# Kernel optimization log

Measured on AMD Instinct MI355X. Metric: run time of the kernel, lower is better.

The kernel has to match this reference:

```python
import jax, jax.numpy as jnp
import numpy as np

B, T, N, F, H, R, E = 32, 8, 150, 16, 32, 4, 16


def _gconv(X, Af, Wf):
    # t-product graph conv (Kilmer t-product = circular conv over relation axis,
    # implemented facewise in the Fourier domain): ifft( fft(adj) @ fft(X) @ fft(W) )
    Xf = jnp.fft.fft(X, axis=-1)                      # [b,n,f,r] complex
    Y = jnp.einsum('nmr,bmfr->bnfr', Af, Xf)          # aggregate over nodes
    Y = jnp.einsum('bnfr,for->bnor', Y, Wf)           # feature transform
    return jnp.fft.ifft(Y, axis=-1).real


def _cell(X, Hs, Af, Wf, Bb):
    # TensorGRUCell. NOTE: faithful to the source, H_tilda reuses conv_hr
    # (conv_hh is defined but never used in the original forward).
    Wxz, Wxr, Wxh, Whz, Whr = Wf
    bz, br, bh = Bb[0], Bb[1], Bb[2]                  # [H,R], broadcasts over [b,n,H,R]
    Z = jax.nn.sigmoid(_gconv(X, Af, Wxz) + _gconv(Hs, Af, Whz) + bz)
    Rg = jax.nn.sigmoid(_gconv(X, Af, Wxr) + _gconv(Hs, Af, Whr) + br)
    Ht = jnp.tanh(_gconv(X, Af, Wxh) + _gconv(Rg * Hs, Af, Whr) + bh)
    return Z * Hs + (1.0 - Z) * Ht


def setup_inputs() -> dict:
    key = jax.random.key(0)
    ks = jax.random.split(key, 16)
    kai = lambda k, shp, fan: (jax.random.normal(k, shp, jnp.float32)
                               * np.float32(np.sqrt(2.0 / fan)))
    d = {}
    d['inputs'] = jax.random.normal(ks[0], (B, T, N, F, R), jnp.float32)
    d['U'] = kai(ks[1], (N, E, R), N)
    # layer 0 (input_dim=F)
    d['Wxz0'] = kai(ks[2], (F, H, R), F)
    d['Wxr0'] = kai(ks[3], (F, H, R), F)
    d['Wxh0'] = kai(ks[4], (F, H, R), F)
    d['Whz0'] = kai(ks[5], (H, H, R), H)
    d['Whr0'] = kai(ks[6], (H, H, R), H)
    d['B0'] = kai(ks[7], (3, H, R), 3)
    # layer 1 (input_dim=H)
    d['Wxz1'] = kai(ks[8], (H, H, R), H)
    d['Wxr1'] = kai(ks[9], (H, H, R), H)
    d['Wxh1'] = kai(ks[10], (H, H, R), H)
    d['Whz1'] = kai(ks[11], (H, H, R), H)
    d['Whr1'] = kai(ks[12], (H, H, R), H)
    d['B1'] = kai(ks[13], (3, H, R), 3)
    return d


def reference(inputs, U, Wxz0, Wxr0, Wxh0, Whz0, Whr0, B0,
              Wxz1, Wxr1, Wxh1, Whz1, Whr1, B1):
    # adaptive adjacency: softmax(relu(tprod(U, U^T)), dim=1)
    Uf = jnp.fft.fft(U, axis=-1)                      # [N,E,R] complex
    A = jnp.fft.ifft(jnp.einsum('ner,mer->nmr', Uf, Uf), axis=-1).real
    adj = jax.nn.softmax(jax.nn.relu(A), axis=1)      # [N,N,R]

    Af = jnp.fft.fft(adj, axis=-1)
    Wf0 = tuple(jnp.fft.fft(w, axis=-1) for w in (Wxz0, Wxr0, Wxh0, Whz0, Whr0))
    Wf1 = tuple(jnp.fft.fft(w, axis=-1) for w in (Wxz1, Wxr1, Wxh1, Whz1, Whr1))

    b, t, n, f, r = inputs.shape
    h = Whz0.shape[0]
    z0 = jnp.zeros((b, n, h, r), inputs.dtype)

    # t = 0: layer1 consumes the *current* layer0 output
    o0 = _cell(inputs[:, 0], z0, Af, Wf0, B0)
    o1 = _cell(o0, z0, Af, Wf1, B1)

    # t > 0: faithful to source, layer1 consumes the *previous timestep's*
    # layer0 output (temp_out[t-1][i-1]) with hidden temp_out[t-1][i].
    def step(carry, Xt):
        p0, p1 = carry
        n0 = _cell(Xt, p0, Af, Wf0, B0)
        n1 = _cell(p0, p1, Af, Wf1, B1)
        return (n0, n1), n1

    Xs = jnp.moveaxis(inputs[:, 1:], 1, 0)            # [T-1,B,N,F,R]
    (c0, c1), ys = jax.lax.scan(step, (o0, o1), Xs)

    out = jnp.concatenate([o1[None], ys], axis=0)     # [T,B,N,H,R]
    out = jnp.moveaxis(out, 0, 1)                     # [B,T,N,H,R]
    h_last = jnp.stack([c0, c1])                      # [L,B,N,H,R]
    return out, h_last
```

## Files before the change

### kernel.cpp

```cpp
#include <hip/hip_runtime.h>
#include <math.h>

#define NN 150
#define BB 32
#define TT 8
#define FF 16
#define HH 32
#define ROWS (NN*BB)
#define NCIN (BB*FF)
#define NCH  (BB*HH)
#define ADJ_LD 160
#define KPAD 68

#define SZ_ADJF (4*NN*ADJ_LD)
#define SZ_WA0  (4*48*32*4)
#define SZ_WA1  (4*64*32*4)
#define SZ_WB   (32*32*4)
#define SZ_STATE (ROWS*HH*4)
#define SZ_PIN  (4*NN*NCIN)

__device__ __forceinline__ float sigmoidf_(float x){ return 1.f/(1.f+expf(-x)); }

__device__ __forceinline__ float comp_of4(float x0, float x1, float x2, float x3, int c) {
  return c==0 ? (x0+x1+x2+x3) : c==1 ? (x0-x2) : c==2 ? (x3-x1) : (x0-x1+x2-x3);
}


__global__ __launch_bounds__(256) void k_adj(const float* __restrict__ U, float* __restrict__ adjF) {
  __shared__ float Ufl[NN*16*4];
  __shared__ float Arow[NN*4];
  __shared__ float red[256];
  __shared__ float mxs[4], isms[4];
  int n = blockIdx.x, tid = threadIdx.x;
  for (int idx = tid; idx < NN*16; idx += 256) {
    const float* s = U + (size_t)idx*4;
    float x0=s[0], x1=s[1], x2=s[2], x3=s[3];
    Ufl[idx*4+0] = x0+x1+x2+x3;
    Ufl[idx*4+1] = x0-x2;
    Ufl[idx*4+2] = x3-x1;
    Ufl[idx*4+3] = x0-x1+x2-x3;
  }
  __syncthreads();
  if (tid < NN) {
    int m = tid;
    float a0=0, ar=0, ai=0, a2=0;
    #pragma unroll
    for (int e = 0; e < 16; ++e) {
      const float* un = &Ufl[(n*16+e)*4];
      const float* um = &Ufl[(m*16+e)*4];
      a0 += un[0]*um[0];
      ar += un[1]*um[1] - un[2]*um[2];
      ai += un[1]*um[2] + un[2]*um[1];
      a2 += un[3]*um[3];
    }
    float r0 = 0.25f*(a0 + 2.f*ar + a2);
    float r1 = 0.25f*(a0 - 2.f*ai - a2);
    float r2 = 0.25f*(a0 - 2.f*ar + a2);
    float r3 = 0.25f*(a0 + 2.f*ai - a2);
    Arow[m*4+0] = fmaxf(r0, 0.f);
    Arow[m*4+1] = fmaxf(r1, 0.f);
    Arow[m*4+2] = fmaxf(r2, 0.f);
    Arow[m*4+3] = fmaxf(r3, 0.f);
  }
  __syncthreads();
  for (int r = 0; r < 4; ++r) {
    float v = (tid < NN) ? Arow[tid*4+r] : -1e30f;
    red[tid] = v; __syncthreads();
    for (int s = 128; s > 0; s >>= 1) { if (tid < s) red[tid] = fmaxf(red[tid], red[tid+s]); __syncthreads(); }
    if (tid == 0) mxs[r] = red[0];
    __syncthreads();
    float e = (tid < NN) ? expf(Arow[tid*4+r] - mxs[r]) : 0.f;
    red[tid] = e; __syncthreads();
    for (int s = 128; s > 0; s >>= 1) { if (tid < s) red[tid] += red[tid+s]; __syncthreads(); }
    if (tid == 0) isms[r] = 1.f / red[0];
    __syncthreads();
    if (tid < NN) Arow[tid*4+r] = e * isms[r];
    __syncthreads();
  }
  if (tid < NN) {
    int m = tid;
    float e0=Arow[m*4+0], e1=Arow[m*4+1], e2=Arow[m*4+2], e3=Arow[m*4+3];
    size_t base = (size_t)n*ADJ_LD + m;
    size_t cs = (size_t)NN*ADJ_LD;
    adjF[base]      = e0+e1+e2+e3;
    adjF[base+cs]   = e0-e2;
    adjF[base+2*cs] = e3-e1;
    adjF[base+3*cs] = e0-e1+e2-e3;
  } else if (tid < ADJ_LD) {
    size_t base = (size_t)n*ADJ_LD + tid;
    size_t cs = (size_t)NN*ADJ_LD;
    adjF[base] = 0.f; adjF[base+cs] = 0.f; adjF[base+2*cs] = 0.f; adjF[base+3*cs] = 0.f;
  }
}

__global__ __launch_bounds__(256) void k_wts(
    const float* __restrict__ Wxz0, const float* __restrict__ Wxr0, const float* __restrict__ Wxh0,
    const float* __restrict__ Whz0, const float* __restrict__ Whr0,
    const float* __restrict__ Wxz1, const float* __restrict__ Wxr1, const float* __restrict__ Wxh1,
    const float* __restrict__ Whz1, const float* __restrict__ Whr1,
    float* __restrict__ WA0p, float* __restrict__ WA1p,
    float* __restrict__ WB0p, float* __restrict__ WB1p) {
  int idx = blockIdx.x*256 + threadIdx.x;
  const float* src = nullptr;
  float* dst; int didx; int c;
  if (idx < SZ_WA0) {
    c = idx / 6144;
    int rem = idx % 6144;
    int k = rem >> 7, og = (rem >> 2) & 31, q = rem & 3;
    if (q == 0) src = (k < FF) ? Wxz0 + ((size_t)k*HH + og)*4 : Whz0 + ((size_t)(k-FF)*HH + og)*4;
    else if (q == 1) src = (k < FF) ? Wxr0 + ((size_t)k*HH + og)*4 : Whr0 + ((size_t)(k-FF)*HH + og)*4;
    else if (q == 2 && k < FF) src = Wxh0 + ((size_t)k*HH + og)*4;
    dst = WA0p; didx = idx;
  } else if (idx < SZ_WA0 + SZ_WA1) {
    int id = idx - SZ_WA0;
    c = id >> 13;
    int rem = id & 8191;
    int k = rem >> 7, og = (rem >> 2) & 31, q = rem & 3;
    if (q == 0) src = (k < HH) ? Wxz1 + ((size_t)k*HH + og)*4 : Whz1 + ((size_t)(k-HH)*HH + og)*4;
    else if (q == 1) src = (k < HH) ? Wxr1 + ((size_t)k*HH + og)*4 : Whr1 + ((size_t)(k-HH)*HH + og)*4;
    else if (q == 2 && k < HH) src = Wxh1 + ((size_t)k*HH + og)*4;
    dst = WA1p; didx = id;
  } else if (idx < SZ_WA0 + SZ_WA1 + SZ_WB) {
    int id = idx - (SZ_WA0 + SZ_WA1);
    int k = id >> 7, o = (id >> 2) & 31;
    c = id & 3;
    src = Whr0 + ((size_t)k*HH + o)*4;
    dst = WB0p; didx = id;
  } else if (idx < SZ_WA0 + SZ_WA1 + 2*SZ_WB) {
    int id = idx - (SZ_WA0 + SZ_WA1 + SZ_WB);
    int k = id >> 7, o = (id >> 2) & 31;
    c = id & 3;
    src = Whr1 + ((size_t)k*HH + o)*4;
    dst = WB1p; didx = id;
  } else return;
  float v0=0,v1=0,v2=0,v3=0;
  if (src) { v0=src[0]; v1=src[1]; v2=src[2]; v3=src[3]; }
  dst[didx] = comp_of4(v0,v1,v2,v3,c);
}

struct AggParams {
  const float* X0; const float* X1; const float* X2;
  float* P0; float* P1; float* P2;
  int ncol0, ncol1, ncol2;
  int base1, base2, njobs, rawt, nb;
};
__global__ __launch_bounds__(256,4) void k_agg(AggParams pr, const float* __restrict__ adjF,
                                               const float* __restrict__ inp) {
  __shared__ float As[4*32*37];
  __shared__ float Xs[4*32*36];
  int bid = blockIdx.x;
  int part = (bid >= pr.nb) ? 1 : 0;
  if (part) bid -= pr.nb;
  const float* X; float* P; int ncol; int tile; bool raw = false;
  if (pr.njobs >= 3 && bid >= pr.base2) { X = pr.X2; P = pr.P2; ncol = pr.ncol2; tile = bid - pr.base2; }
  else if (pr.njobs >= 2 && bid >= pr.base1) { X = pr.X1; P = pr.P1; ncol = pr.ncol1; tile = bid - pr.base1; }
  else { X = pr.X0; P = pr.P0; ncol = pr.ncol0; tile = bid; raw = (pr.rawt >= 0); }
  P += (size_t)part * 4 * NN * ncol;
  int kbeg = part ? 96 : 0;
  int kend = part ? NN : 96;
  int n0 = (tile % 5) * 32;
  int col0 = (tile / 5) * 32;
  int tid = threadIdx.x;
  int ti = tid & 31, tj = tid >> 5;
  int j0 = tj * 4;
  float a0[4]={}, aR[4]={}, aI[4]={}, a2v[4]={};

  float4 pa[4];
  float4 px[4];

  #define LOAD_A(K0)                                                         \
    _Pragma("unroll")                                                        \
    for (int u = 0; u < 4; ++u) {                                            \
      int e = tid + u*256;                                                   \
      int c = e >> 8, rem = e & 255, i = rem >> 3, kq = rem & 7;             \
      int nn_ = n0 + i;                                                      \
      pa[u] = make_float4(0,0,0,0);                                          \
      if (nn_ < NN) pa[u] = *(const float4*)(adjF + ((size_t)c*NN + nn_)*ADJ_LD + (K0) + kq*4); \
    }
  #define STORE_A()                                                          \
    _Pragma("unroll")                                                        \
    for (int u = 0; u < 4; ++u) {                                            \
      int e = tid + u*256;                                                   \
      int c = e >> 8, rem = e & 255, i = rem >> 3, kq = rem & 7;             \
      As[(c*32 + kq*4+0)*37 + i] = pa[u].x;                                  \
      As[(c*32 + kq*4+1)*37 + i] = pa[u].y;                                  \
      As[(c*32 + kq*4+2)*37 + i] = pa[u].z;                                  \
      As[(c*32 + kq*4+3)*37 + i] = pa[u].w;                                  \
    }
  #define LOAD_X(K0)                                                         \
    if (raw) {                                                               \
      int q = tid & 7, kk = tid >> 3;                                        \
      int mm = (K0) + kk;                                                    \
      int col = col0 + q*4;                                                  \
      int b = col >> 4, f = col & 15;                                        \
      px[0]=px[1]=px[2]=px[3]=make_float4(0,0,0,0);                          \
      if (mm < NN) {                                                         \
        const float* s = inp + (((size_t)(b*TT + pr.rawt)*NN + mm)*FF + f)*4;\
        px[0] = *(const float4*)(s+0);                                       \
        px[1] = *(const float4*)(s+4);                                       \
        px[2] = *(const float4*)(s+8);                                       \
        px[3] = *(const float4*)(s+12);                                      \
      }                                                                      \
    } else {                                                                 \
      _Pragma("unroll")                                                      \
      for (int u = 0; u < 4; ++u) {                                          \
        int e = tid + u*256;                                                 \
        int c = e >> 8, rem = e & 255, kk = rem >> 3, q = rem & 7;           \
        int mm = (K0) + kk;                                                  \
        px[u] = make_float4(0,0,0,0);                                        \
        if (mm < NN) px[u] = *(const float4*)(X + ((size_t)c*NN + mm)*ncol + col0 + q*4); \
      }                                                                      \
    }
  #define STORE_X()                                                          \
    if (raw) {                                                               \
      int q = tid & 7, kk = tid >> 3;                                        \
      float4 r0 = px[0], r1 = px[1], r2 = px[2], r3 = px[3];                 \
      float4 w;                                                              \
      w = make_float4(r0.x+r0.y+r0.z+r0.w, r1.x+r1.y+r1.z+r1.w, r2.x+r2.y+r2.z+r2.w, r3.x+r3.y+r3.z+r3.w); \
      *(float4*)&Xs[(0*32+kk)*36 + q*4] = w;                                 \
      w = make_float4(r0.x-r0.z, r1.x-r1.z, r2.x-r2.z, r3.x-r3.z);           \
      *(float4*)&Xs[(1*32+kk)*36 + q*4] = w;                                 \
      w = make_float4(r0.w-r0.y, r1.w-r1.y, r2.w-r2.y, r3.w-r3.y);           \
      *(float4*)&Xs[(2*32+kk)*36 + q*4] = w;                                 \
      w = make_float4(r0.x-r0.y+r0.z-r0.w, r1.x-r1.y+r1.z-r1.w, r2.x-r2.y+r2.z-r2.w, r3.x-r3.y+r3.z-r3.w); \
      *(float4*)&Xs[(3*32+kk)*36 + q*4] = w;                                 \
    } else {                                                                 \
      _Pragma("unroll")                                                      \
      for (int u = 0; u < 4; ++u) {                                          \
        int e = tid + u*256;                                                 \
        int c = e >> 8, rem = e & 255, kk = rem >> 3, q = rem & 7;           \
        *(float4*)&Xs[(c*32+kk)*36 + q*4] = px[u];                           \
      }                                                                      \
    }

  LOAD_A(kbeg)
  LOAD_X(kbeg)
  for (int k0 = kbeg; k0 < kend; k0 += 32) {
    STORE_A()
    STORE_X()
    __syncthreads();
    int k0n = k0 + 32;
    if (k0n < kend) {
      LOAD_A(k0n)
      LOAD_X(k0n)
    }
    #pragma unroll 4
    for (int k = 0; k < 32; ++k) {
      float A0 = As[(0*32+k)*37 + ti];
      float A1 = As[(1*32+k)*37 + ti];
      float A2 = As[(2*32+k)*37 + ti];
      float A3 = As[(3*32+k)*37 + ti];
      float4 x0 = *(float4*)&Xs[(0*32+k)*36 + j0];
      float4 x1 = *(float4*)&Xs[(1*32+k)*36 + j0];
      float4 x2 = *(float4*)&Xs[(2*32+k)*36 + j0];
      float4 x3 = *(float4*)&Xs[(3*32+k)*36 + j0];
      float X0v[4]={x0.x,x0.y,x0.z,x0.w}, X1v[4]={x1.x,x1.y,x1.z,x1.w};
      float X2v[4]={x2.x,x2.y,x2.z,x2.w}, X3v[4]={x3.x,x3.y,x3.z,x3.w};
      #pragma unroll
      for (int j = 0; j < 4; ++j) {
        a0[j] += A0*X0v[j];
        aR[j] += A1*X1v[j] - A2*X2v[j];
        aI[j] += A1*X2v[j] + A2*X1v[j];
        a2v[j] += A3*X3v[j];
      }
    }
    __syncthreads();
  }
  int nn_ = n0 + ti;
  if (nn_ < NN) {
    size_t cs = (size_t)NN*ncol;
    size_t rb = (size_t)nn_*ncol + col0 + j0;
    *(float4*)&P[rb]      = make_float4(a0[0],a0[1],a0[2],a0[3]);
    *(float4*)&P[rb+cs]   = make_float4(aR[0],aR[1],aR[2],aR[3]);
    *(float4*)&P[rb+2*cs] = make_float4(aI[0],aI[1],aI[2],aI[3]);
    *(float4*)&P[rb+3*cs] = make_float4(a2v[0],a2v[1],a2v[2],a2v[3]);
  }
}

struct FAJob {
  const float* Px;
  const float* Ph;
  const float* W;
  const float* bias;
  const float* hprev;
  float* Z; float* T1; float* Mf;
  int zh;
};
struct FAParams { FAJob j[2]; };

template<int KTOT, int KX>
__device__ __forceinline__ void fusedA_body(const FAJob& jb, float* Ps, float* Ws) {
  const int row0 = blockIdx.x * 16;
  const int tid = threadIdx.x;
  const int og = tid & 31;
  const int rg = tid >> 5;
  const int r0 = rg*2, r1 = rg*2 + 1;
  const size_t psx = (size_t)4*ROWS*KX;
  const size_t psh = (size_t)4*ROWS*HH;
  constexpr int K4 = KTOT/4;
  for (int e = tid; e < 16*4*K4; e += 256) {
    int k4 = e % K4; int c = (e / K4) & 3; int r = e / (K4*4);
    int k = k4*4;
    int row = row0 + r;
    float4 v;
    if (k < KX) {
      const float* a = &jb.Px[((size_t)c*ROWS + row)*KX + k];
      float4 va = *(const float4*)a;
      float4 vb = *(const float4*)(a + psx);
      v = make_float4(va.x+vb.x, va.y+vb.y, va.z+vb.z, va.w+vb.w);
    } else if (jb.zh) {
      v = make_float4(0,0,0,0);
    } else {
      const float* a = &jb.Ph[((size_t)c*ROWS + row)*HH + (k - KX)];
      float4 va = *(const float4*)a;
      float4 vb = *(const float4*)(a + psh);
      v = make_float4(va.x+vb.x, va.y+vb.y, va.z+vb.z, va.w+vb.w);
    }
    *(float4*)&Ps[(r*4 + c)*KPAD + k] = v;
  }
  float acc0[2][3]={{0,0,0},{0,0,0}}, accR[2][3]={{0,0,0},{0,0,0}};
  float accI[2][3]={{0,0,0},{0,0,0}}, acc2[2][3]={{0,0,0},{0,0,0}};
  constexpr int NCHK = KTOT/16;
  const float4* Wg = (const float4*)jb.W;
  for (int cc = 0; cc < NCHK; ++cc) {
    __syncthreads();
    #pragma unroll
    for (int u = 0; u < 8; ++u) {
      int f = tid + u*256;
      int c = f >> 9, rem = f & 511;
      float4 v = Wg[((size_t)c*KTOT + cc*16)*32 + rem];
      *(float4*)&Ws[((size_t)c*512 + rem)*4] = v;
    }
    __syncthreads();
    #pragma unroll 4
    for (int kk = 0; kk < 16; ++kk) {
      int k = cc*16 + kk;
      float p0a = Ps[(r0*4+0)*KPAD + k];
      float p1a = Ps[(r0*4+1)*KPAD + k];
      float p2a = Ps[(r0*4+2)*KPAD + k];
      float p3a = Ps[(r0*4+3)*KPAD + k];
      float p0b = Ps[(r1*4+0)*KPAD + k];
      float p1b = Ps[(r1*4+1)*KPAD + k];
      float p2b = Ps[(r1*4+2)*KPAD + k];
      float p3b = Ps[(r1*4+3)*KPAD + k];
      float4 w0 = *(float4*)&Ws[((0*16+kk)*32+og)*4];
      float4 w1 = *(float4*)&Ws[((1*16+kk)*32+og)*4];
      float4 w2 = *(float4*)&Ws[((2*16+kk)*32+og)*4];
      float4 w3 = *(float4*)&Ws[((3*16+kk)*32+og)*4];
      float W0v[3]={w0.x,w0.y,w0.z}, W1v[3]={w1.x,w1.y,w1.z};
      float W2v[3]={w2.x,w2.y,w2.z}, W3v[3]={w3.x,w3.y,w3.z};
      #pragma unroll
      for (int q = 0; q < 3; ++q) {
        acc0[0][q] += p0a*W0v[q];
        acc0[1][q] += p0b*W0v[q];
        accR[0][q] += p1a*W1v[q] - p2a*W2v[q];
        accR[1][q] += p1b*W1v[q] - p2b*W2v[q];
        accI[0][q] += p1a*W2v[q] + p2a*W1v[q];
        accI[1][q] += p1b*W2v[q] + p2b*W1v[q];
        acc2[0][q] += p3a*W3v[q];
        acc2[1][q] += p3b*W3v[q];
      }
    }
  }
  const float* bz = jb.bias + (0*HH + og)*4;
  const float* br = jb.bias + (1*HH + og)*4;
  const float* bh = jb.bias + (2*HH + og)*4;
  float bzv[4] = {bz[0],bz[1],bz[2],bz[3]};
  float brv[4] = {br[0],br[1],br[2],br[3]};
  float bhv[4] = {bh[0],bh[1],bh[2],bh[3]};
  #pragma unroll
  for (int rr = 0; rr < 2; ++rr) {
    int row = row0 + rg*2 + rr;
    float ys[3][4];
    #pragma unroll
    for (int q = 0; q < 3; ++q) {
      float Y0 = acc0[rr][q], Yr = accR[rr][q], Yi = accI[rr][q], Y2 = acc2[rr][q];
      ys[q][0] = 0.25f*(Y0 + 2.f*Yr + Y2);
      ys[q][1] = 0.25f*(Y0 - 2.f*Yi - Y2);
      ys[q][2] = 0.25f*(Y0 - 2.f*Yr + Y2);
      ys[q][3] = 0.25f*(Y0 + 2.f*Yi - Y2);
    }
    float4 z = make_float4(sigmoidf_(ys[0][0]+bzv[0]), sigmoidf_(ys[0][1]+bzv[1]),
                           sigmoidf_(ys[0][2]+bzv[2]), sigmoidf_(ys[0][3]+bzv[3]));
    *(float4*)&jb.Z[((size_t)row*HH + og)*4] = z;
    float4 hp = make_float4(0,0,0,0);
    if (!jb.zh) hp = *(const float4*)&jb.hprev[((size_t)row*HH + og)*4];
    float m0 = sigmoidf_(ys[1][0]+brv[0]) * hp.x;
    float m1 = sigmoidf_(ys[1][1]+brv[1]) * hp.y;
    float m2 = sigmoidf_(ys[1][2]+brv[2]) * hp.z;
    float m3 = sigmoidf_(ys[1][3]+brv[3]) * hp.w;
    size_t mb = (size_t)row*HH + og;
    size_t cs = (size_t)ROWS*HH;
    jb.Mf[mb]      = m0+m1+m2+m3;
    jb.Mf[mb+cs]   = m0-m2;
    jb.Mf[mb+2*cs] = m3-m1;
    jb.Mf[mb+3*cs] = m0-m1+m2-m3;
    float4 tv = make_float4(ys[2][0]+bhv[0], ys[2][1]+bhv[1], ys[2][2]+bhv[2], ys[2][3]+bhv[3]);
    *(float4*)&jb.T1[((size_t)row*HH + og)*4] = tv;
  }
}

__global__ __launch_bounds__(256,3) void k_fusedA_both(FAParams pr) {
  __shared__ float Ps[16*4*KPAD];
  __shared__ float Ws[8192];
  if (blockIdx.y == 0) fusedA_body<48,16>(pr.j[0], Ps, Ws);
  else                 fusedA_body<64,32>(pr.j[1], Ps, Ws);
}
__global__ __launch_bounds__(256,3) void k_fusedA_L0(FAParams pr) {
  __shared__ float Ps[16*4*KPAD];
  __shared__ float Ws[8192];
  fusedA_body<48,16>(pr.j[0], Ps, Ws);
}
__global__ __launch_bounds__(256,3) void k_fusedA_L1(FAParams pr) {
  __shared__ float Ps[16*4*KPAD];
  __shared__ float Ws[8192];
  fusedA_body<64,32>(pr.j[1], Ps, Ws);
}

struct FBJob {
  const float* Pm; const float* W; const float* T1; const float* Z;
  float* h; float* hf; float* outp; float* hlast;
  int t, zh, wout;
};
struct FBParams { FBJob j[2]; };
__global__ __launch_bounds__(256,4) void k_fusedB(FBParams pr) {
  __shared__ float Ps[16*32*4];
  __shared__ float Ws[32*32*4];
  FBJob jb = pr.j[blockIdx.y];
  int row0 = blockIdx.x * 16;
  int tid = threadIdx.x;
  int rg = tid >> 5, o = tid & 31;
  int r0 = rg*2, r1 = r0 + 1;
  float acc0[2]={0,0}, accR[2]={0,0}, accI[2]={0,0}, acc2[2]={0,0};
  if (!jb.zh) {
    #pragma unroll
    for (int u = 0; u < 4; ++u) {
      int f = tid + u*256;
      ((float4*)Ws)[f] = ((const float4*)jb.W)[f];
    }
    const size_t psh = (size_t)4*ROWS*HH;
    #pragma unroll
    for (int u = 0; u < 2; ++u) {
      int e = tid + u*256;
      int r = e >> 5, k = e & 31;
      int row = row0 + r;
      float4 v;
      float* vv = (float*)&v;
      #pragma unroll
      for (int c = 0; c < 4; ++c) {
        size_t ix = ((size_t)c*ROWS + row)*HH + k;
        vv[c] = jb.Pm[ix] + jb.Pm[ix + psh];
      }
      *(float4*)&Ps[(r*32 + k)*4] = v;
    }
    __syncthreads();
    #pragma unroll 8
    for (int k = 0; k < 32; ++k) {
      float4 pA = *(const float4*)&Ps[(r0*32 + k)*4];
      float4 pB = *(const float4*)&Ps[(r1*32 + k)*4];
      float4 w  = *(const float4*)&Ws[(k*32 + o)*4];
      acc0[0] += pA.x*w.x;  acc0[1] += pB.x*w.x;
      accR[0] += pA.y*w.y - pA.z*w.z;  accR[1] += pB.y*w.y - pB.z*w.z;
      accI[0] += pA.y*w.z + pA.z*w.y;  accI[1] += pB.y*w.z + pB.z*w.y;
      acc2[0] += pA.w*w.w;  acc2[1] += pB.w*w.w;
    }
  }
  #pragma unroll
  for (int rr = 0; rr < 2; ++rr) {
    int row = row0 + rg*2 + rr;
    float y0 = 0.25f*(acc0[rr] + 2.f*accR[rr] + acc2[rr]);
    float y1 = 0.25f*(acc0[rr] - 2.f*accI[rr] - acc2[rr]);
    float y2 = 0.25f*(acc0[rr] - 2.f*accR[rr] + acc2[rr]);
    float y3 = 0.25f*(acc0[rr] + 2.f*accI[rr] - acc2[rr]);
    float4 t1 = *(const float4*)&jb.T1[((size_t)row*HH + o)*4];
    float h0v = tanhf(t1.x + y0);
    float h1v = tanhf(t1.y + y1);
    float h2v = tanhf(t1.z + y2);
    float h3v = tanhf(t1.w + y3);
    float4 z = *(const float4*)&jb.Z[((size_t)row*HH + o)*4];
    float4 hp = make_float4(0,0,0,0);
    if (!jb.zh) hp = *(const float4*)&jb.h[((size_t)row*HH + o)*4];
    float n0v = z.x*hp.x + (1.f-z.x)*h0v;
    float n1v = z.y*hp.y + (1.f-z.y)*h1v;
    float n2v = z.z*hp.z + (1.f-z.z)*h2v;
    float n3v = z.w*hp.w + (1.f-z.w)*h3v;
    *(float4*)&jb.h[((size_t)row*HH + o)*4] = make_float4(n0v,n1v,n2v,n3v);
    size_t hb = (size_t)row*HH + o, cs = (size_t)ROWS*HH;
    jb.hf[hb]      = n0v+n1v+n2v+n3v;
    jb.hf[hb+cs]   = n0v-n2v;
    jb.hf[hb+2*cs] = n3v-n1v;
    jb.hf[hb+3*cs] = n0v-n1v+n2v-n3v;
    int n = row >> 5, b = row & 31;
    if (jb.wout) {
      float* dst = jb.outp + (((size_t)b*TT + jb.t)*NN + n)*(HH*4) + o*4;
      *(float4*)dst = make_float4(n0v,n1v,n2v,n3v);
    }
    if (jb.hlast) {
      float* dst = jb.hlast + ((size_t)(b*NN + n))*(HH*4) + o*4;
      *(float4*)dst = make_float4(n0v,n1v,n2v,n3v);
    }
  }
}

extern "C" void kernel_launch(void* const* d_in, const int* in_sizes, int n_in,
                              void* d_out, int out_size, void* d_ws, size_t ws_size,
                              hipStream_t stream) {
  const float* inp  = (const float*)d_in[0];
  const float* U    = (const float*)d_in[1];
  const float* Wxz0 = (const float*)d_in[2];
  const float* Wxr0 = (const float*)d_in[3];
  const float* Wxh0 = (const float*)d_in[4];
  const float* Whz0 = (const float*)d_in[5];
  const float* Whr0 = (const float*)d_in[6];
  const float* B0   = (const float*)d_in[7];
  const float* Wxz1 = (const float*)d_in[8];
  const float* Wxr1 = (const float*)d_in[9];
  const float* Wxh1 = (const float*)d_in[10];
  const float* Whz1 = (const float*)d_in[11];
  const float* Whr1 = (const float*)d_in[12];
  const float* B1   = (const float*)d_in[13];
  float* out = (float*)d_out;

  float* ws = (float*)d_ws;
  float* ADJF = ws;  ws += SZ_ADJF;
  float* WA0  = ws;  ws += SZ_WA0;
  float* WA1  = ws;  ws += SZ_WA1;
  float* WB0  = ws;  ws += SZ_WB;
  float* WB1  = ws;  ws += SZ_WB;
  float* H0   = ws;  ws += SZ_STATE;
  float* H1   = ws;  ws += SZ_STATE;
  float* H0F  = ws;  ws += SZ_STATE;
  float* H1F  = ws;  ws += SZ_STATE;
  float* PIN  = ws;  ws += 2*SZ_PIN;
  float* PH0  = ws;  ws += 2*SZ_STATE;
  float* PH1  = ws;  ws += 2*SZ_STATE;
  float* PM0  = ws;  ws += 2*SZ_STATE;
  float* PM1  = ws;  ws += 2*SZ_STATE;
  float* M0F  = ws;  ws += SZ_STATE;
  float* M1F  = ws;  ws += SZ_STATE;
  float* Z0   = ws;  ws += SZ_STATE;
  float* Z1   = ws;  ws += SZ_STATE;
  float* T10  = ws;  ws += SZ_STATE;
  float* T11  = ws;  ws += SZ_STATE;

  k_adj<<<NN, 256, 0, stream>>>(U, ADJF);
  k_wts<<<(SZ_WA0+SZ_WA1+2*SZ_WB+255)/256, 256, 0, stream>>>(
      Wxz0,Wxr0,Wxh0,Whz0,Whr0,Wxz1,Wxr1,Wxh1,Whz1,Whr1,WA0,WA1,WB0,WB1);

  {
    AggParams p; p.X0=nullptr; p.P0=PIN; p.ncol0=NCIN;
    p.X1=nullptr; p.P1=nullptr; p.ncol1=0; p.X2=nullptr; p.P2=nullptr; p.ncol2=0;
    p.base1=0; p.base2=0; p.njobs=1; p.rawt=0; p.nb=80;
    k_agg<<<160, 256, 0, stream>>>(p, ADJF, inp);
  }
  {
    FAParams p;
    p.j[0] = FAJob{PIN, nullptr, WA0, B0, nullptr, Z0, T10, M0F, 1};
    p.j[1] = p.j[0];
    k_fusedA_L0<<<dim3(300,1), 256, 0, stream>>>(p);
  }
  {
    FBParams p;
    p.j[0] = FBJob{nullptr, WB0, T10, Z0, H0, H0F, nullptr, nullptr, 0, 1, 0};
    p.j[1] = p.j[0];
    k_fusedB<<<dim3(300,1), 256, 0, stream>>>(p);
  }
  {
    AggParams p; p.X0=H0F; p.P0=PH0; p.ncol0=NCH;
    p.X1=nullptr; p.P1=nullptr; p.ncol1=0; p.X2=nullptr; p.P2=nullptr; p.ncol2=0;
    p.base1=0; p.base2=0; p.njobs=1; p.rawt=-1; p.nb=160;
    k_agg<<<320, 256, 0, stream>>>(p, ADJF, inp);
  }
  {
    FAParams p;
    p.j[0] = FAJob{PH0, nullptr, WA1, B1, nullptr, Z1, T11, M1F, 1};
    p.j[1] = p.j[0];
    k_fusedA_L1<<<dim3(300,1), 256, 0, stream>>>(p);
  }
  {
    FBParams p;
    p.j[0] = FBJob{nullptr, WB1, T11, Z1, H1, H1F, out, nullptr, 0, 1, 1};
    p.j[1] = p.j[0];
    k_fusedB<<<dim3(300,1), 256, 0, stream>>>(p);
  }

  float* hlast0 = out + (size_t)BB*TT*NN*HH*4;
  float* hlast1 = hlast0 + (size_t)BB*NN*HH*4;
  for (int t = 1; t < TT; ++t) {
    {
      AggParams p;
      p.X0=nullptr; p.P0=PIN; p.ncol0=NCIN;
      p.X1=H0F; p.P1=PH0; p.ncol1=NCH;
      p.X2=H1F; p.P2=PH1; p.ncol2=NCH;
      p.base1=80; p.base2=240; p.njobs=3; p.rawt=t; p.nb=400;
      k_agg<<<800, 256, 0, stream>>>(p, ADJF, inp);
    }
    {
      FAParams p;
      p.j[0] = FAJob{PIN, PH0, WA0, B0, H0, Z0, T10, M0F, 0};
      p.j[1] = FAJob{PH0, PH1, WA1, B1, H1, Z1, T11, M1F, 0};
      k_fusedA_both<<<dim3(300,2), 256, 0, stream>>>(p);
    }
    {
      AggParams p;
      p.X0=M0F; p.P0=PM0; p.ncol0=NCH;
      p.X1=M1F; p.P1=PM1; p.ncol1=NCH;
      p.X2=nullptr; p.P2=nullptr; p.ncol2=0;
      p.base1=160; p.base2=0; p.njobs=2; p.rawt=-1; p.nb=320;
      k_agg<<<640, 256, 0, stream>>>(p, ADJF, inp);
    }
    {
      int last = (t == TT-1);
      FBParams p;
      p.j[0] = FBJob{PM0, WB0, T10, Z0, H0, H0F, nullptr, last ? hlast0 : nullptr, t, 0, 0};
      p.j[1] = FBJob{PM1, WB1, T11, Z1, H1, H1F, out,     last ? hlast1 : nullptr, t, 0, 1};
      k_fusedB<<<dim3(300,2), 256, 0, stream>>>(p);
    }
  }
}
```

Baseline: 846.2 us.

## Fuse recurrent timestep kernels into persistent megakernel with grid barriers

Replaces the roughly thirty small per-timestep launches with one persistent kernel. Its blocks loop over work units for each stage and synchronise through atomic-counter grid barriers. The input aggregation for all timesteps is hoisted into one up-front kernel, and the adjacency and weight preprocessing kernels are merged into one launch. The aim is to remove launch overhead and the idle tails between dependent stages. In exchange it relies on all blocks being co-resident: the grid is sized from an occupancy query, and a miscount would deadlock. Spin-wait barriers also add their own latency at each stage.

```diff
diff --git a/kernel.cpp b/kernel.cpp
--- a/kernel.cpp
+++ b/kernel.cpp
@@ -26,81 +26,83 @@
 }
 
 
-__global__ __launch_bounds__(256) void k_adj(const float* __restrict__ U, float* __restrict__ adjF) {
-  __shared__ float Ufl[NN*16*4];
-  __shared__ float Arow[NN*4];
-  __shared__ float red[256];
-  __shared__ float mxs[4], isms[4];
-  int n = blockIdx.x, tid = threadIdx.x;
-  for (int idx = tid; idx < NN*16; idx += 256) {
-    const float* s = U + (size_t)idx*4;
-    float x0=s[0], x1=s[1], x2=s[2], x3=s[3];
-    Ufl[idx*4+0] = x0+x1+x2+x3;
-    Ufl[idx*4+1] = x0-x2;
-    Ufl[idx*4+2] = x3-x1;
-    Ufl[idx*4+3] = x0-x1+x2-x3;
-  }
-  __syncthreads();
-  if (tid < NN) {
-    int m = tid;
-    float a0=0, ar=0, ai=0, a2=0;
-    #pragma unroll
-    for (int e = 0; e < 16; ++e) {
-      const float* un = &Ufl[(n*16+e)*4];
-      const float* um = &Ufl[(m*16+e)*4];
-      a0 += un[0]*um[0];
-      ar += un[1]*um[1] - un[2]*um[2];
-      ai += un[1]*um[2] + un[2]*um[1];
-      a2 += un[3]*um[3];
-    }
-    float r0 = 0.25f*(a0 + 2.f*ar + a2);
-    float r1 = 0.25f*(a0 - 2.f*ai - a2);
-    float r2 = 0.25f*(a0 - 2.f*ar + a2);
-    float r3 = 0.25f*(a0 + 2.f*ai - a2);
-    Arow[m*4+0] = fmaxf(r0, 0.f);
-    Arow[m*4+1] = fmaxf(r1, 0.f);
-    Arow[m*4+2] = fmaxf(r2, 0.f);
-    Arow[m*4+3] = fmaxf(r3, 0.f);
-  }
-  __syncthreads();
-  for (int r = 0; r < 4; ++r) {
-    float v = (tid < NN) ? Arow[tid*4+r] : -1e30f;
-    red[tid] = v; __syncthreads();
-    for (int s = 128; s > 0; s >>= 1) { if (tid < s) red[tid] = fmaxf(red[tid], red[tid+s]); __syncthreads(); }
-    if (tid == 0) mxs[r] = red[0];
-    __syncthreads();
-    float e = (tid < NN) ? expf(Arow[tid*4+r] - mxs[r]) : 0.f;
-    red[tid] = e; __syncthreads();
-    for (int s = 128; s > 0; s >>= 1) { if (tid < s) red[tid] += red[tid+s]; __syncthreads(); }
-    if (tid == 0) isms[r] = 1.f / red[0];
-    __syncthreads();
-    if (tid < NN) Arow[tid*4+r] = e * isms[r];
-    __syncthreads();
-  }
-  if (tid < NN) {
-    int m = tid;
-    float e0=Arow[m*4+0], e1=Arow[m*4+1], e2=Arow[m*4+2], e3=Arow[m*4+3];
-    size_t base = (size_t)n*ADJ_LD + m;
-    size_t cs = (size_t)NN*ADJ_LD;
-    adjF[base]      = e0+e1+e2+e3;
-    adjF[base+cs]   = e0-e2;
-    adjF[base+2*cs] = e3-e1;
-    adjF[base+3*cs] = e0-e1+e2-e3;
-  } else if (tid < ADJ_LD) {
-    size_t base = (size_t)n*ADJ_LD + tid;
-    size_t cs = (size_t)NN*ADJ_LD;
-    adjF[base] = 0.f; adjF[base+cs] = 0.f; adjF[base+2*cs] = 0.f; adjF[base+3*cs] = 0.f;
-  }
-}
-
-__global__ __launch_bounds__(256) void k_wts(
+__global__ __launch_bounds__(256) void k_pre(
+    const float* __restrict__ U, float* __restrict__ adjF,
     const float* __restrict__ Wxz0, const float* __restrict__ Wxr0, const float* __restrict__ Wxh0,
     const float* __restrict__ Whz0, const float* __restrict__ Whr0,
     const float* __restrict__ Wxz1, const float* __restrict__ Wxr1, const float* __restrict__ Wxh1,
     const float* __restrict__ Whz1, const float* __restrict__ Whr1,
     float* __restrict__ WA0p, float* __restrict__ WA1p,
     float* __restrict__ WB0p, float* __restrict__ WB1p) {
-  int idx = blockIdx.x*256 + threadIdx.x;
+  __shared__ float Ufl[NN*16*4];
+  __shared__ float Arow[NN*4];
+  __shared__ float red[256];
+  __shared__ float mxs[4], isms[4];
+  int tid = threadIdx.x;
+  if (blockIdx.x < NN) {
+    int n = blockIdx.x;
+    for (int idx = tid; idx < NN*16; idx += 256) {
+      const float* s = U + (size_t)idx*4;
+      float x0=s[0], x1=s[1], x2=s[2], x3=s[3];
+      Ufl[idx*4+0] = x0+x1+x2+x3;
+      Ufl[idx*4+1] = x0-x2;
+      Ufl[idx*4+2] = x3-x1;
+      Ufl[idx*4+3] = x0-x1+x2-x3;
+    }
+    __syncthreads();
+    if (tid < NN) {
+      int m = tid;
+      float a0=0, ar=0, ai=0, a2=0;
+      #pragma unroll
+      for (int e = 0; e < 16; ++e) {
+        const float* un = &Ufl[(n*16+e)*4];
+        const float* um = &Ufl[(m*16+e)*4];
+        a0 += un[0]*um[0];
+        ar += un[1]*um[1] - un[2]*um[2];
+        ai += un[1]*um[2] + un[2]*um[1];
+        a2 += un[3]*um[3];
+      }
+      float r0 = 0.25f*(a0 + 2.f*ar + a2);
+      float r1 = 0.25f*(a0 - 2.f*ai - a2);
+      float r2 = 0.25f*(a0 - 2.f*ar + a2);
+      float r3 = 0.25f*(a0 + 2.f*ai - a2);
+      Arow[m*4+0] = fmaxf(r0, 0.f);
+      Arow[m*4+1] = fmaxf(r1, 0.f);
+      Arow[m*4+2] = fmaxf(r2, 0.f);
+      Arow[m*4+3] = fmaxf(r3, 0.f);
+    }
+    __syncthreads();
+    for (int r = 0; r < 4; ++r) {
+      float v = (tid < NN) ? Arow[tid*4+r] : -1e30f;
+      red[tid] = v; __syncthreads();
+      for (int s = 128; s > 0; s >>= 1) { if (tid < s) red[tid] = fmaxf(red[tid], red[tid+s]); __syncthreads(); }
+      if (tid == 0) mxs[r] = red[0];
+      __syncthreads();
+      float e = (tid < NN) ? expf(Arow[tid*4+r] - mxs[r]) : 0.f;
+      red[tid] = e; __syncthreads();
+      for (int s = 128; s > 0; s >>= 1) { if (tid < s) red[tid] += red[tid+s]; __syncthreads(); }
+      if (tid == 0) isms[r] = 1.f / red[0];
+      __syncthreads();
+      if (tid < NN) Arow[tid*4+r] = e * isms[r];
+      __syncthreads();
+    }
+    if (tid < NN) {
+      int m = tid;
+      float e0=Arow[m*4+0], e1=Arow[m*4+1], e2=Arow[m*4+2], e3=Arow[m*4+3];
+      size_t base = (size_t)n*ADJ_LD + m;
+      size_t cs = (size_t)NN*ADJ_LD;
+      adjF[base]      = e0+e1+e2+e3;
+      adjF[base+cs]   = e0-e2;
+      adjF[base+2*cs] = e3-e1;
+      adjF[base+3*cs] = e0-e1+e2-e3;
+    } else if (tid < ADJ_LD) {
+      size_t base = (size_t)n*ADJ_LD + tid;
+      size_t cs = (size_t)NN*ADJ_LD;
+      adjF[base] = 0.f; adjF[base+cs] = 0.f; adjF[base+2*cs] = 0.f; adjF[base+3*cs] = 0.f;
+    }
+    return;
+  }
+  int idx = (blockIdx.x - NN)*256 + tid;
   const float* src = nullptr;
   float* dst; int didx; int c;
   if (idx < SZ_WA0) {
@@ -138,35 +140,21 @@
   dst[didx] = comp_of4(v0,v1,v2,v3,c);
 }
 
-struct AggParams {
-  const float* X0; const float* X1; const float* X2;
-  float* P0; float* P1; float* P2;
-  int ncol0, ncol1, ncol2;
-  int base1, base2, njobs, rawt, nb;
-};
-__global__ __launch_bounds__(256,4) void k_agg(AggParams pr, const float* __restrict__ adjF,
-                                               const float* __restrict__ inp) {
-  __shared__ float As[4*32*37];
-  __shared__ float Xs[4*32*36];
-  int bid = blockIdx.x;
-  int part = (bid >= pr.nb) ? 1 : 0;
-  if (part) bid -= pr.nb;
-  const float* X; float* P; int ncol; int tile; bool raw = false;
-  if (pr.njobs >= 3 && bid >= pr.base2) { X = pr.X2; P = pr.P2; ncol = pr.ncol2; tile = bid - pr.base2; }
-  else if (pr.njobs >= 2 && bid >= pr.base1) { X = pr.X1; P = pr.P1; ncol = pr.ncol1; tile = bid - pr.base1; }
-  else { X = pr.X0; P = pr.P0; ncol = pr.ncol0; tile = bid; raw = (pr.rawt >= 0); }
-  P += (size_t)part * 4 * NN * ncol;
+template<bool RAW>
+__device__ __forceinline__ void agg_body(const float* __restrict__ adjF,
+                                         const float* __restrict__ X,
+                                         const float* __restrict__ inp,
+                                         float* __restrict__ P, int ncol,
+                                         int tile, int part, int rawt,
+                                         float* As, float* Xs, int tid) {
   int kbeg = part ? 96 : 0;
   int kend = part ? NN : 96;
   int n0 = (tile % 5) * 32;
   int col0 = (tile / 5) * 32;
-  int tid = threadIdx.x;
   int ti = tid & 31, tj = tid >> 5;
   int j0 = tj * 4;
   float a0[4]={}, aR[4]={}, aI[4]={}, a2v[4]={};
-
-  float4 pa[4];
-  float4 px[4];
+  float4 pa[4], px[4];
 
   #define LOAD_A(K0)                                                         \
     _Pragma("unroll")                                                        \
@@ -188,14 +176,14 @@
       As[(c*32 + kq*4+3)*37 + i] = pa[u].w;                                  \
     }
   #define LOAD_X(K0)                                                         \
-    if (raw) {                                                               \
+    if (RAW) {                                                               \
       int q = tid & 7, kk = tid >> 3;                                        \
       int mm = (K0) + kk;                                                    \
       int col = col0 + q*4;                                                  \
       int b = col >> 4, f = col & 15;                                        \
       px[0]=px[1]=px[2]=px[3]=make_float4(0,0,0,0);                          \
       if (mm < NN) {                                                         \
-        const float* s = inp + (((size_t)(b*TT + pr.rawt)*NN + mm)*FF + f)*4;\
+        const float* s = inp + (((size_t)(b*TT + rawt)*NN + mm)*FF + f)*4;   \
         px[0] = *(const float4*)(s+0);                                       \
         px[1] = *(const float4*)(s+4);                                       \
         px[2] = *(const float4*)(s+8);                                       \
@@ -212,7 +200,7 @@
       }                                                                      \
     }
   #define STORE_X()                                                          \
-    if (raw) {                                                               \
+    if (RAW) {                                                               \
       int q = tid & 7, kk = tid >> 3;                                        \
       float4 r0 = px[0], r1 = px[1], r2 = px[2], r3 = px[3];                 \
       float4 w;                                                              \
@@ -266,6 +254,10 @@
     }
     __syncthreads();
   }
+  #undef LOAD_A
+  #undef STORE_A
+  #undef LOAD_X
+  #undef STORE_X
   int nn_ = n0 + ti;
   if (nn_ < NN) {
     size_t cs = (size_t)NN*ncol;
@@ -275,6 +267,17 @@
     *(float4*)&P[rb+2*cs] = make_float4(aI[0],aI[1],aI[2],aI[3]);
     *(float4*)&P[rb+3*cs] = make_float4(a2v[0],a2v[1],a2v[2],a2v[3]);
   }
+}
+
+__global__ __launch_bounds__(256,4) void k_aggIN(const float* __restrict__ adjF,
+                                                 const float* __restrict__ inp,
+                                                 float* __restrict__ PIN) {
+  __shared__ float As[4736];
+  __shared__ float Xs[4608];
+  int u = blockIdx.x;
+  int t = u / 160, rem = u % 160, part = rem / 80, tile = rem % 80;
+  float* P = PIN + (size_t)t*2*SZ_PIN + (size_t)part*SZ_PIN;
+  agg_body<true>(adjF, nullptr, inp, P, NCIN, tile, part, t, As, Xs, threadIdx.x);
 }
 
 struct FAJob {
@@ -286,12 +289,11 @@
   float* Z; float* T1; float* Mf;
   int zh;
 };
-struct FAParams { FAJob j[2]; };
 
 template<int KTOT, int KX>
-__device__ __forceinline__ void fusedA_body(const FAJob& jb, float* Ps, float* Ws) {
-  const int row0 = blockIdx.x * 16;
-  const int tid = threadIdx.x;
+__device__ __forceinline__ void fusedA_unit(const FAJob& jb, float* Ps, float* Ws, int unit, int tid) {
+  __syncthreads();
+  const int row0 = unit * 16;
   const int og = tid & 31;
   const int rg = tid >> 5;
   const int r0 = rg*2, r1 = rg*2 + 1;
@@ -400,35 +402,15 @@
   }
 }
 
-__global__ __launch_bounds__(256,3) void k_fusedA_both(FAParams pr) {
-  __shared__ float Ps[16*4*KPAD];
-  __shared__ float Ws[8192];
-  if (blockIdx.y == 0) fusedA_body<48,16>(pr.j[0], Ps, Ws);
-  else                 fusedA_body<64,32>(pr.j[1], Ps, Ws);
-}
-__global__ __launch_bounds__(256,3) void k_fusedA_L0(FAParams pr) {
-  __shared__ float Ps[16*4*KPAD];
-  __shared__ float Ws[8192];
-  fusedA_body<48,16>(pr.j[0], Ps, Ws);
-}
-__global__ __launch_bounds__(256,3) void k_fusedA_L1(FAParams pr) {
-  __shared__ float Ps[16*4*KPAD];
-  __shared__ float Ws[8192];
-  fusedA_body<64,32>(pr.j[1], Ps, Ws);
-}
-
 struct FBJob {
   const float* Pm; const float* W; const float* T1; const float* Z;
   float* h; float* hf; float* outp; float* hlast;
   int t, zh, wout;
 };
-struct FBParams { FBJob j[2]; };
-__global__ __launch_bounds__(256,4) void k_fusedB(FBParams pr) {
-  __shared__ float Ps[16*32*4];
-  __shared__ float Ws[32*32*4];
-  FBJob jb = pr.j[blockIdx.y];
-  int row0 = blockIdx.x * 16;
-  int tid = threadIdx.x;
+
+__device__ __forceinline__ void fusedB_unit(const FBJob& jb, float* Ps, float* Ws, int unit, int tid) {
+  __syncthreads();
+  int row0 = unit * 16;
   int rg = tid >> 5, o = tid & 31;
   int r0 = rg*2, r1 = r0 + 1;
   float acc0[2]={0,0}, accR[2]={0,0}, accI[2]={0,0}, acc2[2]={0,0};
@@ -502,6 +484,104 @@
   }
 }
 
+__device__ __forceinline__ void gbar(int* cnt, int idx, int nblk) {
+  __syncthreads();
+  if (threadIdx.x == 0) {
+    __threadfence();
+    atomicAdd(&cnt[idx], 1);
+    while (__hip_atomic_load(&cnt[idx], __ATOMIC_RELAXED, __HIP_MEMORY_SCOPE_AGENT) < nblk) {
+      __builtin_amdgcn_s_sleep(2);
+    }
+    __threadfence();
+  }
+  __syncthreads();
+}
+
+struct MegaParams {
+  const float* adjF; const float* PIN;
+  const float* WA0; const float* WA1; const float* WB0; const float* WB1;
+  const float* B0; const float* B1;
+  float* H0; float* H1; float* H0F; float* H1F;
+  float* PH0; float* PH1; float* PM0; float* PM1;
+  float* M0F; float* M1F; float* Z0; float* Z1; float* T10; float* T11;
+  float* out; float* hlast0; float* hlast1;
+  int* cnt; int nblk;
+};
+
+__global__ __launch_bounds__(256,3) void k_mega(MegaParams mp) {
+  __shared__ float smem[12544];
+  const int tid = threadIdx.x;
+  const int bid = blockIdx.x;
+  const int gsz = gridDim.x;
+  int bslot = 0;
+
+  for (int u = bid; u < 300; u += gsz) {
+    FAJob jb{mp.PIN, nullptr, mp.WA0, mp.B0, nullptr, mp.Z0, mp.T10, mp.M0F, 1};
+    fusedA_unit<48,16>(jb, smem, smem+4352, u, tid);
+  }
+  gbar(mp.cnt, bslot++, mp.nblk);
+  for (int u = bid; u < 300; u += gsz) {
+    FBJob jb{nullptr, mp.WB0, mp.T10, mp.Z0, mp.H0, mp.H0F, nullptr, nullptr, 0, 1, 0};
+    fusedB_unit(jb, smem, smem+2048, u, tid);
+  }
+  gbar(mp.cnt, bslot++, mp.nblk);
+  for (int u = bid; u < 320; u += gsz) {
+    int part = u / 160, tile = u % 160;
+    agg_body<false>(mp.adjF, mp.H0F, nullptr, mp.PH0 + (size_t)part*SZ_STATE, NCH, tile, part, -1,
+                    smem, smem+4736, tid);
+  }
+  gbar(mp.cnt, bslot++, mp.nblk);
+  for (int u = bid; u < 300; u += gsz) {
+    FAJob jb{mp.PH0, nullptr, mp.WA1, mp.B1, nullptr, mp.Z1, mp.T11, mp.M1F, 1};
+    fusedA_unit<64,32>(jb, smem, smem+4352, u, tid);
+  }
+  gbar(mp.cnt, bslot++, mp.nblk);
+  for (int u = bid; u < 300; u += gsz) {
+    FBJob jb{nullptr, mp.WB1, mp.T11, mp.Z1, mp.H1, mp.H1F, mp.out, nullptr, 0, 1, 1};
+    fusedB_unit(jb, smem, smem+2048, u, tid);
+  }
+  gbar(mp.cnt, bslot++, mp.nblk);
+
+  for (int t = 1; t < TT; ++t) {
+    const float* PINt = mp.PIN + (size_t)t * 2 * SZ_PIN;
+    for (int u = bid; u < 640; u += gsz) {
+      int job = u / 320, rem = u % 320, part = rem / 160, tile = rem % 160;
+      const float* X = job ? mp.H1F : mp.H0F;
+      float* P = (job ? mp.PH1 : mp.PH0) + (size_t)part*SZ_STATE;
+      agg_body<false>(mp.adjF, X, nullptr, P, NCH, tile, part, -1, smem, smem+4736, tid);
+    }
+    gbar(mp.cnt, bslot++, mp.nblk);
+    for (int u = bid; u < 600; u += gsz) {
+      if (u < 300) {
+        FAJob jb{PINt, mp.PH0, mp.WA0, mp.B0, mp.H0, mp.Z0, mp.T10, mp.M0F, 0};
+        fusedA_unit<48,16>(jb, smem, smem+4352, u, tid);
+      } else {
+        FAJob jb{mp.PH0, mp.PH1, mp.WA1, mp.B1, mp.H1, mp.Z1, mp.T11, mp.M1F, 0};
+        fusedA_unit<64,32>(jb, smem, smem+4352, u-300, tid);
+      }
+    }
+    gbar(mp.cnt, bslot++, mp.nblk);
+    for (int u = bid; u < 640; u += gsz) {
+      int job = u / 320, rem = u % 320, part = rem / 160, tile = rem % 160;
+      const float* X = job ? mp.M1F : mp.M0F;
+      float* P = (job ? mp.PM1 : mp.PM0) + (size_t)part*SZ_STATE;
+      agg_body<false>(mp.adjF, X, nullptr, P, NCH, tile, part, -1, smem, smem+4736, tid);
+    }
+    gbar(mp.cnt, bslot++, mp.nblk);
+    int last = (t == TT-1);
+    for (int u = bid; u < 600; u += gsz) {
+      if (u < 300) {
+        FBJob jb{mp.PM0, mp.WB0, mp.T10, mp.Z0, mp.H0, mp.H0F, nullptr, last ? mp.hlast0 : nullptr, t, 0, 0};
+        fusedB_unit(jb, smem, smem+2048, u, tid);
+      } else {
+        FBJob jb{mp.PM1, mp.WB1, mp.T11, mp.Z1, mp.H1, mp.H1F, mp.out, last ? mp.hlast1 : nullptr, t, 0, 1};
+        fusedB_unit(jb, smem, smem+2048, u-300, tid);
+      }
+    }
+    if (!last) gbar(mp.cnt, bslot++, mp.nblk);
+  }
+}
+
 extern "C" void kernel_launch(void* const* d_in, const int* in_sizes, int n_in,
                               void* d_out, int out_size, void* d_ws, size_t ws_size,
                               hipStream_t stream) {
@@ -531,7 +611,7 @@
   float* H1   = ws;  ws += SZ_STATE;
   float* H0F  = ws;  ws += SZ_STATE;
   float* H1F  = ws;  ws += SZ_STATE;
-  float* PIN  = ws;  ws += 2*SZ_PIN;
+  float* PIN  = ws;  ws += (size_t)TT*2*SZ_PIN;
   float* PH0  = ws;  ws += 2*SZ_STATE;
   float* PH1  = ws;  ws += 2*SZ_STATE;
   float* PM0  = ws;  ws += 2*SZ_STATE;
@@ -542,79 +622,32 @@
   float* Z1   = ws;  ws += SZ_STATE;
   float* T10  = ws;  ws += SZ_STATE;
   float* T11  = ws;  ws += SZ_STATE;
-
-  k_adj<<<NN, 256, 0, stream>>>(U, ADJF);
-  k_wts<<<(SZ_WA0+SZ_WA1+2*SZ_WB+255)/256, 256, 0, stream>>>(
-      Wxz0,Wxr0,Wxh0,Whz0,Whr0,Wxz1,Wxr1,Wxh1,Whz1,Whr1,WA0,WA1,WB0,WB1);
-
-  {
-    AggParams p; p.X0=nullptr; p.P0=PIN; p.ncol0=NCIN;
-    p.X1=nullptr; p.P1=nullptr; p.ncol1=0; p.X2=nullptr; p.P2=nullptr; p.ncol2=0;
-    p.base1=0; p.base2=0; p.njobs=1; p.rawt=0; p.nb=80;
-    k_agg<<<160, 256, 0, stream>>>(p, ADJF, inp);
-  }
-  {
-    FAParams p;
-    p.j[0] = FAJob{PIN, nullptr, WA0, B0, nullptr, Z0, T10, M0F, 1};
-    p.j[1] = p.j[0];
-    k_fusedA_L0<<<dim3(300,1), 256, 0, stream>>>(p);
-  }
-  {
-    FBParams p;
-    p.j[0] = FBJob{nullptr, WB0, T10, Z0, H0, H0F, nullptr, nullptr, 0, 1, 0};
-    p.j[1] = p.j[0];
-    k_fusedB<<<dim3(300,1), 256, 0, stream>>>(p);
-  }
-  {
-    AggParams p; p.X0=H0F; p.P0=PH0; p.ncol0=NCH;
-    p.X1=nullptr; p.P1=nullptr; p.ncol1=0; p.X2=nullptr; p.P2=nullptr; p.ncol2=0;
-    p.base1=0; p.base2=0; p.njobs=1; p.rawt=-1; p.nb=160;
-    k_agg<<<320, 256, 0, stream>>>(p, ADJF, inp);
-  }
-  {
-    FAParams p;
-    p.j[0] = FAJob{PH0, nullptr, WA1, B1, nullptr, Z1, T11, M1F, 1};
-    p.j[1] = p.j[0];
-    k_fusedA_L1<<<dim3(300,1), 256, 0, stream>>>(p);
-  }
-  {
-    FBParams p;
-    p.j[0] = FBJob{nullptr, WB1, T11, Z1, H1, H1F, out, nullptr, 0, 1, 1};
-    p.j[1] = p.j[0];
-    k_fusedB<<<dim3(300,1), 256, 0, stream>>>(p);
-  }
-
-  float* hlast0 = out + (size_t)BB*TT*NN*HH*4;
-  float* hlast1 = hlast0 + (size_t)BB*NN*HH*4;
-  for (int t = 1; t < TT; ++t) {
-    {
-      AggParams p;
-      p.X0=nullptr; p.P0=PIN; p.ncol0=NCIN;
-      p.X1=H0F; p.P1=PH0; p.ncol1=NCH;
-      p.X2=H1F; p.P2=PH1; p.ncol2=NCH;
-      p.base1=80; p.base2=240; p.njobs=3; p.rawt=t; p.nb=400;
-      k_agg<<<800, 256, 0, stream>>>(p, ADJF, inp);
-    }
-    {
-      FAParams p;
-      p.j[0] = FAJob{PIN, PH0, WA0, B0, H0, Z0, T10, M0F, 0};
-      p.j[1] = FAJob{PH0, PH1, WA1, B1, H1, Z1, T11, M1F, 0};
-      k_fusedA_both<<<dim3(300,2), 256, 0, stream>>>(p);
-    }
-    {
-      AggParams p;
-      p.X0=M0F; p.P0=PM0; p.ncol0=NCH;
-      p.X1=M1F; p.P1=PM1; p.ncol1=NCH;
-      p.X2=nullptr; p.P2=nullptr; p.ncol2=0;
-      p.base1=160; p.base2=0; p.njobs=2; p.rawt=-1; p.nb=320;
-      k_agg<<<640, 256, 0, stream>>>(p, ADJF, inp);
-    }
-    {
-      int last = (t == TT-1);
-      FBParams p;
-      p.j[0] = FBJob{PM0, WB0, T10, Z0, H0, H0F, nullptr, last ? hlast0 : nullptr, t, 0, 0};
-      p.j[1] = FBJob{PM1, WB1, T11, Z1, H1, H1F, out,     last ? hlast1 : nullptr, t, 0, 1};
-      k_fusedB<<<dim3(300,2), 256, 0, stream>>>(p);
-    }
-  }
-}
+  int*   CNT  = (int*)ws; ws += 64;
+
+  hipMemsetAsync(CNT, 0, 64*sizeof(int), stream);
+
+  k_pre<<<NN + (SZ_WA0+SZ_WA1+2*SZ_WB+255)/256, 256, 0, stream>>>(
+      U, ADJF, Wxz0,Wxr0,Wxh0,Whz0,Whr0, Wxz1,Wxr1,Wxh1,Whz1,Whr1, WA0,WA1,WB0,WB1);
+
+  k_aggIN<<<TT*2*80, 256, 0, stream>>>(ADJF, inp, PIN);
+
+  int nbPerCU = 0;
+  if (hipOccupancyMaxActiveBlocksPerMultiprocessor(&nbPerCU, k_mega, 256, 0) != hipSuccess || nbPerCU <= 0)
+    nbPerCU = 2;
+  int grid = nbPerCU * 256;
+  if (grid > 640) grid = 640;
+
+  MegaParams mp;
+  mp.adjF = ADJF; mp.PIN = PIN;
+  mp.WA0 = WA0; mp.WA1 = WA1; mp.WB0 = WB0; mp.WB1 = WB1;
+  mp.B0 = B0; mp.B1 = B1;
+  mp.H0 = H0; mp.H1 = H1; mp.H0F = H0F; mp.H1F = H1F;
+  mp.PH0 = PH0; mp.PH1 = PH1; mp.PM0 = PM0; mp.PM1 = PM1;
+  mp.M0F = M0F; mp.M1F = M1F; mp.Z0 = Z0; mp.Z1 = Z1; mp.T10 = T10; mp.T11 = T11;
+  mp.out = out;
+  mp.hlast0 = out + (size_t)BB*TT*NN*HH*4;
+  mp.hlast1 = mp.hlast0 + (size_t)BB*NN*HH*4;
+  mp.cnt = CNT; mp.nblk = grid;
+
+  k_mega<<<grid, 256, 0, stream>>>(mp);
+}
```

Measured after the change: 2.099 ms. +148.1%, slower.
